# Kernel optimization log

Hardware: AMD Instinct MI355X
Metric: run time of the kernel (lower is better)

## Reference

```python
import jax, jax.numpy as jnp
import numpy as np

T, H, E, I, SI, TOP_K = 4096, 2048, 16, 1024, 4096, 1


def setup_inputs() -> dict:
    key = jax.random.key(0)
    ks = jax.random.split(key, 8)
    s_h = 1.0 / np.sqrt(H)
    s_i = 1.0 / np.sqrt(I)
    s_si = 1.0 / np.sqrt(SI)
    return {
        "hidden_states": jax.random.normal(ks[0], (T, H), jnp.float32),
        "router_w": jax.random.normal(ks[1], (E, H), jnp.float32) * s_h,
        "w_gate": jax.random.normal(ks[2], (E, H, I), jnp.float32) * s_h,
        "w_up": jax.random.normal(ks[3], (E, H, I), jnp.float32) * s_h,
        "w_down": jax.random.normal(ks[4], (E, I, H), jnp.float32) * s_i,
        "ws_gate": jax.random.normal(ks[5], (H, SI), jnp.float32) * s_h,
        "ws_up": jax.random.normal(ks[6], (H, SI), jnp.float32) * s_h,
        "ws_down": jax.random.normal(ks[7], (SI, H), jnp.float32) * s_si,
    }


def reference(hidden_states, router_w, w_gate, w_up, w_down, ws_gate, ws_up, ws_down):
    x = hidden_states  # [T, H]
    # Router: logits -> top-k -> sigmoid weights (Llama4RenormalizeMoeRoutingMethod)
    logits = jnp.einsum("th,eh->te", x, router_w)              # [T, E]
    top_vals, top_idx = jax.lax.top_k(logits, TOP_K)            # [T, K]
    weights = jax.nn.sigmoid(top_vals)                          # [T, K]
    # dispatch[t, e] = router weight if expert e selected for token t, else 0
    onehot = jax.nn.one_hot(top_idx, E, dtype=x.dtype)          # [T, K, E]
    dispatch = jnp.einsum("tke,tk->te", onehot, weights)        # [T, E]
    # Routed experts: router weight applied on input (commutes through the
    # linear gate/up projections as a per-(t,e) scalar applied before SiLU).
    g = jnp.einsum("th,ehi->tei", x, w_gate) * dispatch[:, :, None]  # [T, E, I]
    u = jnp.einsum("th,ehi->tei", x, w_up) * dispatch[:, :, None]    # [T, E, I]
    act = jax.nn.silu(g) * u                                          # [T, E, I]
    # Unselected experts contribute exactly 0 (act==0 there), so summing over
    # E in the down projection is the combine step.
    routed = jnp.einsum("tei,eih->th", act, w_down)             # [T, H]
    # Shared expert (SiLU-gated MLP on the unscaled hidden states)
    shared = (jax.nn.silu(x @ ws_gate) * (x @ ws_up)) @ ws_down  # [T, H]
    return shared + routed
```

## Files before the change

kernel.cpp:

```cpp
#include <hip/hip_runtime.h>
#include <hip/hip_bf16.h>

typedef unsigned short u16;
typedef unsigned int   u32;
typedef __attribute__((ext_vector_type(8))) short short8;
typedef __attribute__((ext_vector_type(4))) float f32x4;

#define T_TOK 4096
#define HDIM  2048
#define NEXP  16
#define IDIM  1024
#define SIDIM 4096
#define RCAP  6144
#define NTIL  48

#define O_WT      0u
#define O_EIDX    16384u
#define O_CNT     32768u
#define O_POS     32832u
#define O_PADOFF  32896u
#define O_TILEEXP 33024u
#define O_TOKROW  33280u
#define O_XBF     65536u
#define O_XSC     (O_XBF  + 2u*T_TOK*HDIM)
#define O_ACTS    (O_XSC  + 2u*RCAP*HDIM)
#define O_ACTR    (O_ACTS + 2u*T_TOK*SIDIM)
#define O_WSGT    (O_ACTR + 2u*RCAP*IDIM)
#define O_WSUT    (O_WSGT + 2u*SIDIM*HDIM)
#define O_WSDT    (O_WSUT + 2u*SIDIM*HDIM)

__device__ __forceinline__ u16 f2b(float f) {
  u32 u = __float_as_uint(f);
  u = (u + 0x7FFFu + ((u >> 16) & 1u)) >> 16;
  return (u16)u;
}

#define GLDS16(g, l) __builtin_amdgcn_global_load_lds( \
    (const __attribute__((address_space(1))) void*)(g), \
    (__attribute__((address_space(3))) void*)(l), 16, 0, 0)
#define BARX() __builtin_amdgcn_s_barrier()
#define SETPRIO(x) __builtin_amdgcn_s_setprio(x)
#define WAITVM(n) asm volatile("s_waitcnt vmcnt(" #n ")" ::: "memory")

__global__ __launch_bounds__(256) void router_k(
    const float* __restrict__ x, const float* __restrict__ rw,
    float* __restrict__ wt, int* __restrict__ eidx, int* __restrict__ cnt,
    u16* __restrict__ xbf) {
  int w = threadIdx.x >> 6, l = threadIdx.x & 63;
  int t = blockIdx.x * 4 + w;
  double acc[NEXP];
#pragma unroll
  for (int e = 0; e < NEXP; ++e) acc[e] = 0.0;
  const float* xp = x + (size_t)t * HDIM;
  u16* xo = xbf + (size_t)t * HDIM;
  for (int hb = 0; hb < HDIM; hb += 256) {
    float4 xv = *(const float4*)(xp + hb + l * 4);
    uint2 o;
    o.x = (u32)f2b(xv.x) | ((u32)f2b(xv.y) << 16);
    o.y = (u32)f2b(xv.z) | ((u32)f2b(xv.w) << 16);
    *(uint2*)(xo + hb + l * 4) = o;
#pragma unroll
    for (int e = 0; e < NEXP; ++e) {
      float4 wv = *(const float4*)(rw + (size_t)e * HDIM + hb + l * 4);
      acc[e] += (double)xv.x * wv.x + (double)xv.y * wv.y
              + (double)xv.z * wv.z + (double)xv.w * wv.w;
    }
  }
#pragma unroll
  for (int e = 0; e < NEXP; ++e) {
    double v = acc[e];
#pragma unroll
    for (int off = 32; off; off >>= 1) v += __shfl_xor(v, off, 64);
    acc[e] = v;
  }
  if (l == 0) {
    double best = acc[0]; int be = 0;
#pragma unroll
    for (int e = 1; e < NEXP; ++e) if (acc[e] > best) { best = acc[e]; be = e; }
    wt[t] = 1.0f / (1.0f + __expf(-(float)best));
    eidx[t] = be;
    atomicAdd(&cnt[be], 1);
  }
}

__global__ void scan_k(const int* __restrict__ cnt, int* __restrict__ pad_off,
                       int* __restrict__ tile_exp, int* __restrict__ pos,
                       int* __restrict__ tok_row) {
  if (threadIdx.x == 0) {
    for (int i = 0; i < 64; ++i) tile_exp[i] = -1;
    int run = 0;
    for (int e = 0; e < NEXP; ++e) {
      pad_off[e] = run;
      int pc = ((cnt[e] + 127) >> 7) << 7;
      for (int tt = run >> 7; tt < (run + pc) >> 7; ++tt) tile_exp[tt] = e;
      run += pc;
      pos[e] = 0;
    }
    pad_off[NEXP] = run;
  }
  for (int i = threadIdx.x; i < RCAP; i += 256) tok_row[i] = -1;
}

__global__ void assign_k(const int* __restrict__ eidx, const int* __restrict__ pad_off,
                         int* __restrict__ pos, int* __restrict__ tok_row) {
  int t = blockIdx.x * 256 + threadIdx.x;
  if (t >= T_TOK) return;
  int e = eidx[t];
  int r = atomicAdd(&pos[e], 1);
  tok_row[pad_off[e] + r] = t;
}

__global__ __launch_bounds__(256) void gather_k(
    const float* __restrict__ x, const float* __restrict__ wt,
    const int* __restrict__ tok_row, u16* __restrict__ xsc) {
  int g = blockIdx.x;
  int tid = threadIdx.x;
  u16* dst = xsc + (size_t)g * HDIM;
  int t = tok_row[g];
  if (t < 0) {
    uint2 z; z.x = 0u; z.y = 0u;
#pragma unroll
    for (int i = 0; i < 2; ++i) *(uint2*)(dst + i * 1024 + tid * 4) = z;
  } else {
    float s = wt[t];
    const float* src = x + (size_t)t * HDIM;
#pragma unroll
    for (int i = 0; i < 2; ++i) {
      int c = i * 1024 + tid * 4;
      float4 v = *(const float4*)(src + c);
      uint2 o;
      o.x = (u32)f2b(v.x * s) | ((u32)f2b(v.y * s) << 16);
      o.y = (u32)f2b(v.z * s) | ((u32)f2b(v.w * s) << 16);
      *(uint2*)(dst + c) = o;
    }
  }
}

__device__ __forceinline__ void conv_tile(
    const float* __restrict__ src, u16* __restrict__ dst, int K, int N,
    int bx, int ky, u32 (*lt)[36], int tid) {
  const int n0 = bx * 64, k0 = ky * 64;
  const int l = tid & 63, w = tid >> 6;
  const float* sp = src + (size_t)(k0 + w * 16) * N + n0 + l;
  u32 p[8];
#pragma unroll
  for (int i = 0; i < 8; ++i) {
    float a = sp[(size_t)(2 * i) * N];
    float b = sp[(size_t)(2 * i + 1) * N];
    p[i] = (u32)f2b(a) | ((u32)f2b(b) << 16);
  }
  *(uint4*)&lt[l][w * 8 + 0] = make_uint4(p[0], p[1], p[2], p[3]);
  *(uint4*)&lt[l][w * 8 + 4] = make_uint4(p[4], p[5], p[6], p[7]);
  __syncthreads();
  const int c = tid & 7, n2 = tid >> 3;
#pragma unroll
  for (int rnd = 0; rnd < 2; ++rnd) {
    int n = n2 + rnd * 32;
    uint4 v = *(const uint4*)&lt[n][c * 4];
    *(uint4*)(dst + (size_t)(n0 + n) * K + k0 + c * 8) = v;
  }
}

__global__ __launch_bounds__(256) void megaconv(
    const float* __restrict__ wsg, const float* __restrict__ wsu,
    const float* __restrict__ wsd, u16* wsgT, u16* wsuT, u16* wsdT) {
  __shared__ u32 lt[64][36];
  int idx = blockIdx.x, tid = threadIdx.x;
  if (idx < 2048) {
    conv_tile(wsg, wsgT, 2048, 4096, idx & 63, idx >> 6, lt, tid);
  } else if (idx < 4096) { idx -= 2048;
    conv_tile(wsu, wsuT, 2048, 4096, idx & 63, idx >> 6, lt, tid);
  } else { idx -= 4096;
    conv_tile(wsd, wsdT, 4096, 2048, idx & 31, idx >> 5, lt, tid);
  }
}


__global__ __launch_bounds__(512, 2) void gu_sh8(
    const u16* __restrict__ A, const u16* __restrict__ Bg, const u16* __restrict__ Bu,
    u16* __restrict__ act) {
  extern __shared__ u16 sm[];
  u16* As  = sm;
  u16* Bsm = sm + 32768;
  const int bid = blockIdx.x;
  const int xcd = bid & 7, bi = bid >> 3;
  const int bx = xcd * 4 + (bi & 3), by = bi >> 2;
  const int m0 = by * 256, c0 = bx * 128;
  const int tid = threadIdx.x, l = tid & 63, wid = tid >> 6;
  const int wm = wid >> 1, wn = wid & 1;

  const int cpos = tid & 3, rr = tid >> 2;
  const int gc = (cpos ^ ((rr >> 1) & 3)) * 8;
  const u16* aS0 = A + (size_t)(m0 + rr) * HDIM + gc;
  const u16* aS1 = A + (size_t)(m0 + 128 + rr) * HDIM + gc;
  const int mat = (rr >> 6) & 1;
  const u16* bbase = mat ? Bu : Bg;
  const u16* bS0 = bbase + (size_t)(c0 + (rr & 63)) * HDIM + gc;
  const u16* bS1 = bbase + (size_t)(c0 + 64 + (rr & 63)) * HDIM + gc;
  const int ld0 = tid * 8, ld1 = (512 + tid) * 8;

#define STA_G(bb, kh, koff) do { \
    GLDS16(aS0 + (koff) + (kh) * 32, As + ((bb) * 2 + (kh)) * 8192 + ld0); \
    GLDS16(aS1 + (koff) + (kh) * 32, As + ((bb) * 2 + (kh)) * 8192 + ld1); } while (0)
#define STB_G(bb, kh, koff) do { \
    GLDS16(bS0 + (koff) + (kh) * 32, Bsm + ((bb) * 2 + (kh)) * 8192 + ld0); \
    GLDS16(bS1 + (koff) + (kh) * 32, Bsm + ((bb) * 2 + (kh)) * 8192 + ld1); } while (0)

  const int fch = ((l >> 4) ^ ((l >> 1) & 3)) * 8;
  int aoff[4], boff[8];
#pragma unroll
  for (int mf = 0; mf < 4; ++mf) aoff[mf] = (wm * 64 + mf * 16 + (l & 15)) * 32 + fch;
#pragma unroll
  for (int i = 0; i < 8; ++i) {
    int v = wn * 128 + (i >> 2) * 64 + (i & 3) * 16 + (l & 15);
    boff[i] = v * 32 + fch;
  }
#define LDA_G(bb, kh) do { const u16* s_ = As + ((bb) * 2 + (kh)) * 8192; \
    af[0] = *(const short8*)(s_ + aoff[0]); af[1] = *(const short8*)(s_ + aoff[1]); \
    af[2] = *(const short8*)(s_ + aoff[2]); af[3] = *(const short8*)(s_ + aoff[3]); } while (0)
#define LDB_G(bb, kh, h, d) do { const u16* s_ = Bsm + ((bb) * 2 + (kh)) * 8192; \
    d[0] = *(const short8*)(s_ + boff[(h) * 4 + 0]); d[1] = *(const short8*)(s_ + boff[(h) * 4 + 1]); \
    d[2] = *(const short8*)(s_ + boff[(h) * 4 + 2]); d[3] = *(const short8*)(s_ + boff[(h) * 4 + 3]); } while (0)
#define MM32_G() do { SETPRIO(1); \
    _Pragma("unroll") for (int mf = 0; mf < 4; ++mf) { \
      _Pragma("unroll") for (int nf = 0; nf < 4; ++nf) \
        acc[mf][nf] = __builtin_amdgcn_mfma_f32_16x16x32_bf16(af[mf], bfrA[nf], acc[mf][nf], 0, 0, 0); \
      _Pragma("unroll") for (int nf = 0; nf < 4; ++nf) \
        acc[mf][4 + nf] = __builtin_amdgcn_mfma_f32_16x16x32_bf16(af[mf], bfrB[nf], acc[mf][4 + nf], 0, 0, 0); \
    } SETPRIO(0); } while (0)

  f32x4 acc[4][8];
#pragma unroll
  for (int i = 0; i < 4; ++i)
#pragma unroll
    for (int j = 0; j < 8; ++j)
#pragma unroll
      for (int r = 0; r < 4; ++r) acc[i][j][r] = 0.0f;
  short8 af[4], bfrA[4], bfrB[4];

  STA_G(0, 0, 0); STB_G(0, 0, 0); STA_G(0, 1, 0); STB_G(0, 1, 0);
  WAITVM(4); BARX();
  const int NT = HDIM / 64;
  for (int t = 0; t < NT - 1; ++t) {
    const int b = t & 1, nb = b ^ 1, kn = (t + 1) * 64;
    LDA_G(b, 0); LDB_G(b, 0, 0, bfrA); LDB_G(b, 0, 1, bfrB);
    STA_G(nb, 0, kn); STB_G(nb, 0, kn);
    MM32_G(); WAITVM(4); BARX();
    LDA_G(b, 1); LDB_G(b, 1, 0, bfrA); LDB_G(b, 1, 1, bfrB);
    STA_G(nb, 1, kn); STB_G(nb, 1, kn);
    MM32_G(); WAITVM(4); BARX();
  }
  { const int b = (NT - 1) & 1;
    LDA_G(b, 0); LDB_G(b, 0, 0, bfrA); LDB_G(b, 0, 1, bfrB);
    MM32_G(); WAITVM(0); BARX();
    LDA_G(b, 1); LDB_G(b, 1, 0, bfrA); LDB_G(b, 1, 1, bfrB);
    MM32_G();
  }
#pragma unroll
  for (int mf = 0; mf < 4; ++mf)
#pragma unroll
    for (int nf = 0; nf < 4; ++nf) {
      int col = c0 + wn * 64 + nf * 16 + (l & 15);
      int rowb = m0 + wm * 64 + mf * 16 + (l >> 4) * 4;
#pragma unroll
      for (int r = 0; r < 4; ++r) {
        float g = acc[mf][nf][r], u = acc[mf][4 + nf][r];
        float s = g / (1.0f + __expf(-g));
        act[(size_t)(rowb + r) * SIDIM + col] = f2b(s * u);
      }
    }
#undef STA_G
#undef STB_G
#undef LDA_G
#undef LDB_G
#undef MM32_G
}

__global__ __launch_bounds__(512, 2) void dn_sh8(
    const u16* __restrict__ A, const u16* __restrict__ B, float* __restrict__ out) {
  extern __shared__ u16 sm[];
  u16* As  = sm;
  u16* Bsm = sm + 32768;
  const int bid = blockIdx.x;
  const int xcd = bid & 7, bi = bid >> 3;
  const int bx = xcd * 2 + (bi & 1), by = bi >> 1;
  const int m0 = by * 256, c0 = bx * 128;
  const int tid = threadIdx.x, l = tid & 63, wid = tid >> 6;
  const int wm = wid >> 1, wn = wid & 1;

  const int cpos = tid & 3, rr = tid >> 2;
  const int gc = (cpos ^ ((rr >> 1) & 3)) * 8;
  const u16* aS0 = A + (size_t)(m0 + rr) * SIDIM + gc;
  const u16* aS1 = A + (size_t)(m0 + 128 + rr) * SIDIM + gc;
  const u16* bS  = B + (size_t)(c0 + rr) * SIDIM + gc;
  const int ld0 = tid * 8, ld1 = (512 + tid) * 8;

#define STA_D(bb, kh, koff) do { \
    GLDS16(aS0 + (koff) + (kh) * 32, As + ((bb) * 2 + (kh)) * 8192 + ld0); \
    GLDS16(aS1 + (koff) + (kh) * 32, As + ((bb) * 2 + (kh)) * 8192 + ld1); } while (0)
#define STB_D(bb, kh, koff) \
    GLDS16(bS + (koff) + (kh) * 32, Bsm + ((bb) * 2 + (kh)) * 4096 + ld0)

  const int fch = ((l >> 4) ^ ((l >> 1) & 3)) * 8;
  int aoff[4], boff[4];
#pragma unroll
  for (int mf = 0; mf < 4; ++mf) aoff[mf] = (wm * 64 + mf * 16 + (l & 15)) * 32 + fch;
#pragma unroll
  for (int i = 0; i < 4; ++i) {
    int v = wn * 64 + (i >> 1) * 32 + (i & 1) * 16 + (l & 15);
    boff[i] = v * 32 + fch;
  }
#define LDA_D(bb, kh) do { const u16* s_ = As + ((bb) * 2 + (kh)) * 8192; \
    af[0] = *(const short8*)(s_ + aoff[0]); af[1] = *(const short8*)(s_ + aoff[1]); \
    af[2] = *(const short8*)(s_ + aoff[2]); af[3] = *(const short8*)(s_ + aoff[3]); } while (0)
#define LDB_D(bb, kh, h, d) do { const u16* s_ = Bsm + ((bb) * 2 + (kh)) * 4096; \
    d[0] = *(const short8*)(s_ + boff[(h) * 2 + 0]); \
    d[1] = *(const short8*)(s_ + boff[(h) * 2 + 1]); } while (0)
#define MM16_D() do { SETPRIO(1); \
    _Pragma("unroll") for (int mf = 0; mf < 4; ++mf) { \
      acc[mf][0] = __builtin_amdgcn_mfma_f32_16x16x32_bf16(af[mf], bfrA[0], acc[mf][0], 0, 0, 0); \
      acc[mf][1] = __builtin_amdgcn_mfma_f32_16x16x32_bf16(af[mf], bfrA[1], acc[mf][1], 0, 0, 0); \
      acc[mf][2] = __builtin_amdgcn_mfma_f32_16x16x32_bf16(af[mf], bfrB[0], acc[mf][2], 0, 0, 0); \
      acc[mf][3] = __builtin_amdgcn_mfma_f32_16x16x32_bf16(af[mf], bfrB[1], acc[mf][3], 0, 0, 0); \
    } SETPRIO(0); } while (0)

  f32x4 acc[4][4];
#pragma unroll
  for (int i = 0; i < 4; ++i)
#pragma unroll
    for (int j = 0; j < 4; ++j)
#pragma unroll
      for (int r = 0; r < 4; ++r) acc[i][j][r] = 0.0f;
  short8 af[4], bfrA[2], bfrB[2];

  STA_D(0, 0, 0); STB_D(0, 0, 0); STA_D(0, 1, 0); STB_D(0, 1, 0);
  WAITVM(3); BARX();
  const int NT = SIDIM / 64;
  for (int t = 0; t < NT - 1; ++t) {
    const int b = t & 1, nb = b ^ 1, kn = (t + 1) * 64;
    LDA_D(b, 0); LDB_D(b, 0, 0, bfrA); LDB_D(b, 0, 1, bfrB);
    STA_D(nb, 0, kn); STB_D(nb, 0, kn);
    MM16_D(); WAITVM(3); BARX();
    LDA_D(b, 1); LDB_D(b, 1, 0, bfrA); LDB_D(b, 1, 1, bfrB);
    STA_D(nb, 1, kn); STB_D(nb, 1, kn);
    MM16_D(); WAITVM(3); BARX();
  }
  { const int b = (NT - 1) & 1;
    LDA_D(b, 0); LDB_D(b, 0, 0, bfrA); LDB_D(b, 0, 1, bfrB);
    MM16_D(); WAITVM(0); BARX();
    LDA_D(b, 1); LDB_D(b, 1, 0, bfrA); LDB_D(b, 1, 1, bfrB);
    MM16_D();
  }
#pragma unroll
  for (int mf = 0; mf < 4; ++mf)
#pragma unroll
    for (int nf = 0; nf < 4; ++nf) {
      int col = c0 + wn * 64 + (nf >> 1) * 32 + (nf & 1) * 16 + (l & 15);
      int rowb = m0 + wm * 64 + mf * 16 + (l >> 4) * 4;
#pragma unroll
      for (int r = 0; r < 4; ++r)
        out[(size_t)(rowb + r) * HDIM + col] = acc[mf][nf][r];
    }
#undef STA_D
#undef STB_D
#undef LDA_D
#undef LDB_D
#undef MM16_D
}

__global__ __launch_bounds__(256) void gu_rf(
    const u16* __restrict__ A, const float* __restrict__ Bg0, const float* __restrict__ Bu0,
    u16* __restrict__ act, const int* __restrict__ tile_exp) {
  __shared__ __align__(16) u16 As[128 * 64];
  __shared__ __align__(16) u16 Bgs[64 * 72];
  __shared__ __align__(16) u16 Bus[64 * 72];
  const int tid = threadIdx.x;
  const int l = tid & 63, w = tid >> 6;
  const int wm = w >> 1, wn = w & 1;
  const int m0 = blockIdx.y * 128, n0 = blockIdx.x * 64;
  int e = tile_exp[blockIdx.y];
  if (e < 0) return;
  size_t eo = (size_t)e * HDIM * IDIM;
  const float* Bg = Bg0 + eo;
  const float* Bu = Bu0 + eo;
  f32x4 accg[4][2], accu[4][2];
#pragma unroll
  for (int i = 0; i < 4; ++i)
#pragma unroll
    for (int j = 0; j < 2; ++j)
#pragma unroll
      for (int r = 0; r < 4; ++r) { accg[i][j][r] = 0.0f; accu[i][j][r] = 0.0f; }
  const u16* Ab = A + (size_t)m0 * HDIM;

  for (int k0 = 0; k0 < HDIM; k0 += 64) {
    __syncthreads();
#pragma unroll
    for (int j = 0; j < 4; ++j) {
      int c = j * 256 + tid, r = c >> 3, cc = c & 7;
      GLDS16(Ab + (size_t)r * HDIM + k0 + ((cc ^ (r & 7)) * 8), &As[c * 8]);
    }
    {
      const float* bp = Bg + (size_t)(k0 + w * 16) * IDIM + n0 + l;
      u16 h[16];
#pragma unroll
      for (int i = 0; i < 16; ++i) h[i] = f2b(bp[(size_t)i * IDIM]);
#pragma unroll
      for (int j = 0; j < 4; ++j) {
        uint2 v; v.x = (u32)h[4*j] | ((u32)h[4*j+1] << 16);
        v.y = (u32)h[4*j+2] | ((u32)h[4*j+3] << 16);
        *(uint2*)&Bgs[l * 72 + w * 16 + j * 4] = v;
      }
      bp = Bu + (size_t)(k0 + w * 16) * IDIM + n0 + l;
#pragma unroll
      for (int i = 0; i < 16; ++i) h[i] = f2b(bp[(size_t)i * IDIM]);
#pragma unroll
      for (int j = 0; j < 4; ++j) {
        uint2 v; v.x = (u32)h[4*j] | ((u32)h[4*j+1] << 16);
        v.y = (u32)h[4*j+2] | ((u32)h[4*j+3] << 16);
        *(uint2*)&Bus[l * 72 + w * 16 + j * 4] = v;
      }
    }
    __syncthreads();
#pragma unroll
    for (int kh = 0; kh < 2; ++kh) {
      const int q = kh * 4 + (l >> 4);
      short8 af[4];
#pragma unroll
      for (int mf = 0; mf < 4; ++mf) {
        int r = wm * 64 + mf * 16 + (l & 15);
        af[mf] = *(const short8*)&As[r * 64 + ((q ^ (r & 7)) * 8)];
      }
      short8 bgf[2], buf2[2];
#pragma unroll
      for (int nf = 0; nf < 2; ++nf) {
        int n = wn * 32 + nf * 16 + (l & 15);
        bgf[nf]  = *(const short8*)&Bgs[n * 72 + q * 8];
        buf2[nf] = *(const short8*)&Bus[n * 72 + q * 8];
      }
#pragma unroll
      for (int mf = 0; mf < 4; ++mf)
#pragma unroll
        for (int nf = 0; nf < 2; ++nf) {
          accg[mf][nf] = __builtin_amdgcn_mfma_f32_16x16x32_bf16(af[mf], bgf[nf],  accg[mf][nf], 0, 0, 0);
          accu[mf][nf] = __builtin_amdgcn_mfma_f32_16x16x32_bf16(af[mf], buf2[nf], accu[mf][nf], 0, 0, 0);
        }
    }
  }
#pragma unroll
  for (int mf = 0; mf < 4; ++mf)
#pragma unroll
    for (int nf = 0; nf < 2; ++nf) {
      int col = n0 + wn * 32 + nf * 16 + (l & 15);
#pragma unroll
      for (int r = 0; r < 4; ++r) {
        int row = m0 + wm * 64 + mf * 16 + (l >> 4) * 4 + r;
        float g = accg[mf][nf][r], u = accu[mf][nf][r];
        float s = g / (1.0f + __expf(-g));
        act[(size_t)row * IDIM + col] = f2b(s * u);
      }
    }
}

__global__ __launch_bounds__(256) void dn_rf(
    const u16* __restrict__ A, const float* __restrict__ B0, float* __restrict__ out,
    const int* __restrict__ tile_exp, const int* __restrict__ tok_row) {
  __shared__ __align__(16) u16 As[128 * 64];
  __shared__ __align__(16) u16 Bs[64 * 72];
  const int tid = threadIdx.x;
  const int l = tid & 63, w = tid >> 6;
  const int wm = w >> 1, wn = w & 1;
  const int m0 = blockIdx.y * 128, n0 = blockIdx.x * 64;
  int e = tile_exp[blockIdx.y];
  if (e < 0) return;
  const float* B = B0 + (size_t)e * IDIM * HDIM;
  f32x4 acc[4][2];
#pragma unroll
  for (int i = 0; i < 4; ++i)
#pragma unroll
    for (int j = 0; j < 2; ++j)
#pragma unroll
      for (int r = 0; r < 4; ++r) acc[i][j][r] = 0.0f;
  const u16* Ab = A + (size_t)m0 * IDIM;

  for (int k0 = 0; k0 < IDIM; k0 += 64) {
    __syncthreads();
#pragma unroll
    for (int j = 0; j < 4; ++j) {
      int c = j * 256 + tid, r = c >> 3, cc = c & 7;
      GLDS16(Ab + (size_t)r * IDIM + k0 + ((cc ^ (r & 7)) * 8), &As[c * 8]);
    }
    {
      const float* bp = B + (size_t)(k0 + w * 16) * HDIM + n0 + l;
      u16 h[16];
#pragma unroll
      for (int i = 0; i < 16; ++i) h[i] = f2b(bp[(size_t)i * HDIM]);
#pragma unroll
      for (int j = 0; j < 4; ++j) {
        uint2 v; v.x = (u32)h[4*j] | ((u32)h[4*j+1] << 16);
        v.y = (u32)h[4*j+2] | ((u32)h[4*j+3] << 16);
        *(uint2*)&Bs[l * 72 + w * 16 + j * 4] = v;
      }
    }
    __syncthreads();
#pragma unroll
    for (int kh = 0; kh < 2; ++kh) {
      const int q = kh * 4 + (l >> 4);
      short8 af[4];
#pragma unroll
      for (int mf = 0; mf < 4; ++mf) {
        int r = wm * 64 + mf * 16 + (l & 15);
        af[mf] = *(const short8*)&As[r * 64 + ((q ^ (r & 7)) * 8)];
      }
      short8 bf[2];
#pragma unroll
      for (int nf = 0; nf < 2; ++nf) {
        int n = wn * 32 + nf * 16 + (l & 15);
        bf[nf] = *(const short8*)&Bs[n * 72 + q * 8];
      }
#pragma unroll
      for (int mf = 0; mf < 4; ++mf)
#pragma unroll
        for (int nf = 0; nf < 2; ++nf)
          acc[mf][nf] = __builtin_amdgcn_mfma_f32_16x16x32_bf16(af[mf], bf[nf], acc[mf][nf], 0, 0, 0);
    }
  }
#pragma unroll
  for (int mf = 0; mf < 4; ++mf)
#pragma unroll
    for (int nf = 0; nf < 2; ++nf) {
      int col = n0 + wn * 32 + nf * 16 + (l & 15);
#pragma unroll
      for (int r = 0; r < 4; ++r) {
        int grow = m0 + wm * 64 + mf * 16 + (l >> 4) * 4 + r;
        int t = tok_row[grow];
        if (t >= 0) out[(size_t)t * HDIM + col] += acc[mf][nf][r];
      }
    }
}

extern "C" void kernel_launch(void* const* d_in, const int* in_sizes, int n_in,
                              void* d_out, int out_size, void* d_ws, size_t ws_size,
                              hipStream_t stream) {
  const float* x   = (const float*)d_in[0];
  const float* rw  = (const float*)d_in[1];
  const float* wg  = (const float*)d_in[2];
  const float* wu  = (const float*)d_in[3];
  const float* wd  = (const float*)d_in[4];
  const float* wsg = (const float*)d_in[5];
  const float* wsu = (const float*)d_in[6];
  const float* wsd = (const float*)d_in[7];
  float* out = (float*)d_out;
  char* ws = (char*)d_ws;

  float* wt     = (float*)(ws + O_WT);
  int* eidx     = (int*)(ws + O_EIDX);
  int* cnt      = (int*)(ws + O_CNT);
  int* pos      = (int*)(ws + O_POS);
  int* pad_off  = (int*)(ws + O_PADOFF);
  int* tile_exp = (int*)(ws + O_TILEEXP);
  int* tok_row  = (int*)(ws + O_TOKROW);
  u16* xbf      = (u16*)(ws + O_XBF);
  u16* xsc      = (u16*)(ws + O_XSC);
  u16* acts     = (u16*)(ws + O_ACTS);
  u16* actr     = (u16*)(ws + O_ACTR);
  u16* wsgT     = (u16*)(ws + O_WSGT);
  u16* wsuT     = (u16*)(ws + O_WSUT);
  u16* wsdT     = (u16*)(ws + O_WSDT);

  hipFuncSetAttribute((const void*)gu_sh8, hipFuncAttributeMaxDynamicSharedMemorySize, 131072);
  hipFuncSetAttribute((const void*)dn_sh8, hipFuncAttributeMaxDynamicSharedMemorySize, 98304);

  hipMemsetAsync(ws + O_CNT, 0, 128, stream);
  megaconv<<<6144, 256, 0, stream>>>(wsg, wsu, wsd, wsgT, wsuT, wsdT);
  router_k<<<T_TOK / 4, 256, 0, stream>>>(x, rw, wt, eidx, cnt, xbf);
  scan_k<<<1, 256, 0, stream>>>(cnt, pad_off, tile_exp, pos, tok_row);
  assign_k<<<T_TOK / 256, 256, 0, stream>>>(eidx, pad_off, pos, tok_row);
  gather_k<<<RCAP, 256, 0, stream>>>(x, wt, tok_row, xsc);

  gu_sh8<<<512, 512, 131072, stream>>>(xbf, wsgT, wsuT, acts);
  gu_rf<<<dim3(IDIM / 64, NTIL), 256, 0, stream>>>(xsc, wg, wu, actr, tile_exp);
  dn_sh8<<<256, 512, 98304, stream>>>(acts, wsdT, out);
  dn_rf<<<dim3(HDIM / 64, NTIL), 256, 0, stream>>>(actr, wd, out, tile_exp, tok_row);
}
```

Measured before the change: 569.9 us.

## Software-pipeline routed expert GEMMs with double-buffered A and register-prefetched B

Both routed-expert kernels, gate/up and down, now double-buffer the A tile in LDS. The fp32 weight loads for the next K-step are issued into registers before the current step's MFMAs, so global latency overlaps with compute instead of sitting between two __syncthreads. Synchronisation uses explicit vmcnt/lgkmcnt waits, raw barriers and sched_barrier, and wave priority is raised around the MFMA block. This costs more LDS and registers per block, which could lower occupancy.

```diff
diff --git a/kernel.cpp b/kernel.cpp
--- a/kernel.cpp
+++ b/kernel.cpp
@@ -41,6 +41,8 @@
 #define BARX() __builtin_amdgcn_s_barrier()
 #define SETPRIO(x) __builtin_amdgcn_s_setprio(x)
 #define WAITVM(n) asm volatile("s_waitcnt vmcnt(" #n ")" ::: "memory")
+#define WAITLGKM0() asm volatile("s_waitcnt lgkmcnt(0)" ::: "memory")
+#define SCHEDB() __builtin_amdgcn_sched_barrier(0)
 
 __global__ __launch_bounds__(256) void router_k(
     const float* __restrict__ x, const float* __restrict__ rw,
@@ -368,10 +370,11 @@
 #undef MM16_D
 }
 
+
 __global__ __launch_bounds__(256) void gu_rf(
     const u16* __restrict__ A, const float* __restrict__ Bg0, const float* __restrict__ Bu0,
     u16* __restrict__ act, const int* __restrict__ tile_exp) {
-  __shared__ __align__(16) u16 As[128 * 64];
+  __shared__ __align__(16) u16 As[2][128 * 64];
   __shared__ __align__(16) u16 Bgs[64 * 72];
   __shared__ __align__(16) u16 Bus[64 * 72];
   const int tid = threadIdx.x;
@@ -381,8 +384,8 @@
   int e = tile_exp[blockIdx.y];
   if (e < 0) return;
   size_t eo = (size_t)e * HDIM * IDIM;
-  const float* Bg = Bg0 + eo;
-  const float* Bu = Bu0 + eo;
+  const float* Bgp = Bg0 + eo + n0 + l;
+  const float* Bup = Bu0 + eo + n0 + l;
   f32x4 accg[4][2], accu[4][2];
 #pragma unroll
   for (int i = 0; i < 4; ++i)
@@ -391,36 +394,39 @@
 #pragma unroll
       for (int r = 0; r < 4; ++r) { accg[i][j][r] = 0.0f; accu[i][j][r] = 0.0f; }
   const u16* Ab = A + (size_t)m0 * HDIM;
-
-  for (int k0 = 0; k0 < HDIM; k0 += 64) {
-    __syncthreads();
-#pragma unroll
-    for (int j = 0; j < 4; ++j) {
-      int c = j * 256 + tid, r = c >> 3, cc = c & 7;
-      GLDS16(Ab + (size_t)r * HDIM + k0 + ((cc ^ (r & 7)) * 8), &As[c * 8]);
-    }
-    {
-      const float* bp = Bg + (size_t)(k0 + w * 16) * IDIM + n0 + l;
-      u16 h[16];
-#pragma unroll
-      for (int i = 0; i < 16; ++i) h[i] = f2b(bp[(size_t)i * IDIM]);
-#pragma unroll
-      for (int j = 0; j < 4; ++j) {
-        uint2 v; v.x = (u32)h[4*j] | ((u32)h[4*j+1] << 16);
-        v.y = (u32)h[4*j+2] | ((u32)h[4*j+3] << 16);
-        *(uint2*)&Bgs[l * 72 + w * 16 + j * 4] = v;
-      }
-      bp = Bu + (size_t)(k0 + w * 16) * IDIM + n0 + l;
-#pragma unroll
-      for (int i = 0; i < 16; ++i) h[i] = f2b(bp[(size_t)i * IDIM]);
-#pragma unroll
-      for (int j = 0; j < 4; ++j) {
-        uint2 v; v.x = (u32)h[4*j] | ((u32)h[4*j+1] << 16);
-        v.y = (u32)h[4*j+2] | ((u32)h[4*j+3] << 16);
-        *(uint2*)&Bus[l * 72 + w * 16 + j * 4] = v;
-      }
-    }
-    __syncthreads();
+  float bg[16], bu[16];
+
+#define STAGE_A_R(bb, k0) do { \
+    _Pragma("unroll") for (int j = 0; j < 4; ++j) { \
+      int c_ = j * 256 + tid, r_ = c_ >> 3, cc_ = c_ & 7; \
+      GLDS16(Ab + (size_t)r_ * HDIM + (k0) + ((cc_ ^ (r_ & 7)) * 8), &As[bb][c_ * 8]); } } while (0)
+#define LOADB_R(k0) do { \
+    _Pragma("unroll") for (int i = 0; i < 16; ++i) { \
+      bg[i] = Bgp[(size_t)((k0) + w * 16 + i) * IDIM]; \
+      bu[i] = Bup[(size_t)((k0) + w * 16 + i) * IDIM]; } } while (0)
+#define WRITEB_R() do { \
+    _Pragma("unroll") for (int j = 0; j < 4; ++j) { \
+      uint2 v_; v_.x = (u32)f2b(bg[4*j]) | ((u32)f2b(bg[4*j+1]) << 16); \
+      v_.y = (u32)f2b(bg[4*j+2]) | ((u32)f2b(bg[4*j+3]) << 16); \
+      *(uint2*)&Bgs[l * 72 + w * 16 + j * 4] = v_; \
+      uint2 u_; u_.x = (u32)f2b(bu[4*j]) | ((u32)f2b(bu[4*j+1]) << 16); \
+      u_.y = (u32)f2b(bu[4*j+2]) | ((u32)f2b(bu[4*j+3]) << 16); \
+      *(uint2*)&Bus[l * 72 + w * 16 + j * 4] = u_; } } while (0)
+
+  STAGE_A_R(0, 0);
+  SCHEDB();
+  LOADB_R(0);
+  WAITVM(32); BARX();
+  const int NT = HDIM / 64;
+  for (int t = 0; t < NT; ++t) {
+    const int b = t & 1, nb = b ^ 1;
+    WRITEB_R();
+    if (t + 1 < NT) {
+      STAGE_A_R(nb, (t + 1) * 64);
+      SCHEDB();
+      LOADB_R((t + 1) * 64);
+    }
+    WAITLGKM0(); BARX();
 #pragma unroll
     for (int kh = 0; kh < 2; ++kh) {
       const int q = kh * 4 + (l >> 4);
@@ -428,7 +434,7 @@
 #pragma unroll
       for (int mf = 0; mf < 4; ++mf) {
         int r = wm * 64 + mf * 16 + (l & 15);
-        af[mf] = *(const short8*)&As[r * 64 + ((q ^ (r & 7)) * 8)];
+        af[mf] = *(const short8*)&As[b][r * 64 + ((q ^ (r & 7)) * 8)];
       }
       short8 bgf[2], buf2[2];
 #pragma unroll
@@ -437,6 +443,7 @@
         bgf[nf]  = *(const short8*)&Bgs[n * 72 + q * 8];
         buf2[nf] = *(const short8*)&Bus[n * 72 + q * 8];
       }
+      SETPRIO(1);
 #pragma unroll
       for (int mf = 0; mf < 4; ++mf)
 #pragma unroll
@@ -444,7 +451,9 @@
           accg[mf][nf] = __builtin_amdgcn_mfma_f32_16x16x32_bf16(af[mf], bgf[nf],  accg[mf][nf], 0, 0, 0);
           accu[mf][nf] = __builtin_amdgcn_mfma_f32_16x16x32_bf16(af[mf], buf2[nf], accu[mf][nf], 0, 0, 0);
         }
-    }
+      SETPRIO(0);
+    }
+    WAITVM(32); BARX();
   }
 #pragma unroll
   for (int mf = 0; mf < 4; ++mf)
@@ -459,12 +468,15 @@
         act[(size_t)row * IDIM + col] = f2b(s * u);
       }
     }
+#undef STAGE_A_R
+#undef LOADB_R
+#undef WRITEB_R
 }
 
 __global__ __launch_bounds__(256) void dn_rf(
     const u16* __restrict__ A, const float* __restrict__ B0, float* __restrict__ out,
     const int* __restrict__ tile_exp, const int* __restrict__ tok_row) {
-  __shared__ __align__(16) u16 As[128 * 64];
+  __shared__ __align__(16) u16 As[2][128 * 64];
   __shared__ __align__(16) u16 Bs[64 * 72];
   const int tid = threadIdx.x;
   const int l = tid & 63, w = tid >> 6;
@@ -472,7 +484,7 @@
   const int m0 = blockIdx.y * 128, n0 = blockIdx.x * 64;
   int e = tile_exp[blockIdx.y];
   if (e < 0) return;
-  const float* B = B0 + (size_t)e * IDIM * HDIM;
+  const float* Bp = B0 + (size_t)e * IDIM * HDIM + n0 + l;
   f32x4 acc[4][2];
 #pragma unroll
   for (int i = 0; i < 4; ++i)
@@ -481,27 +493,35 @@
 #pragma unroll
       for (int r = 0; r < 4; ++r) acc[i][j][r] = 0.0f;
   const u16* Ab = A + (size_t)m0 * IDIM;
-
-  for (int k0 = 0; k0 < IDIM; k0 += 64) {
-    __syncthreads();
-#pragma unroll
-    for (int j = 0; j < 4; ++j) {
-      int c = j * 256 + tid, r = c >> 3, cc = c & 7;
-      GLDS16(Ab + (size_t)r * IDIM + k0 + ((cc ^ (r & 7)) * 8), &As[c * 8]);
-    }
-    {
-      const float* bp = B + (size_t)(k0 + w * 16) * HDIM + n0 + l;
-      u16 h[16];
-#pragma unroll
-      for (int i = 0; i < 16; ++i) h[i] = f2b(bp[(size_t)i * HDIM]);
-#pragma unroll
-      for (int j = 0; j < 4; ++j) {
-        uint2 v; v.x = (u32)h[4*j] | ((u32)h[4*j+1] << 16);
-        v.y = (u32)h[4*j+2] | ((u32)h[4*j+3] << 16);
-        *(uint2*)&Bs[l * 72 + w * 16 + j * 4] = v;
-      }
-    }
-    __syncthreads();
+  float bb[16];
+
+#define STAGE_A_D(bbuf, k0) do { \
+    _Pragma("unroll") for (int j = 0; j < 4; ++j) { \
+      int c_ = j * 256 + tid, r_ = c_ >> 3, cc_ = c_ & 7; \
+      GLDS16(Ab + (size_t)r_ * IDIM + (k0) + ((cc_ ^ (r_ & 7)) * 8), &As[bbuf][c_ * 8]); } } while (0)
+#define LOADB_D(k0) do { \
+    _Pragma("unroll") for (int i = 0; i < 16; ++i) \
+      bb[i] = Bp[(size_t)((k0) + w * 16 + i) * HDIM]; } while (0)
+#define WRITEB_D() do { \
+    _Pragma("unroll") for (int j = 0; j < 4; ++j) { \
+      uint2 v_; v_.x = (u32)f2b(bb[4*j]) | ((u32)f2b(bb[4*j+1]) << 16); \
+      v_.y = (u32)f2b(bb[4*j+2]) | ((u32)f2b(bb[4*j+3]) << 16); \
+      *(uint2*)&Bs[l * 72 + w * 16 + j * 4] = v_; } } while (0)
+
+  STAGE_A_D(0, 0);
+  SCHEDB();
+  LOADB_D(0);
+  WAITVM(16); BARX();
+  const int NT = IDIM / 64;
+  for (int t = 0; t < NT; ++t) {
+    const int b = t & 1, nb = b ^ 1;
+    WRITEB_D();
+    if (t + 1 < NT) {
+      STAGE_A_D(nb, (t + 1) * 64);
+      SCHEDB();
+      LOADB_D((t + 1) * 64);
+    }
+    WAITLGKM0(); BARX();
 #pragma unroll
     for (int kh = 0; kh < 2; ++kh) {
       const int q = kh * 4 + (l >> 4);
@@ -509,7 +529,7 @@
 #pragma unroll
       for (int mf = 0; mf < 4; ++mf) {
         int r = wm * 64 + mf * 16 + (l & 15);
-        af[mf] = *(const short8*)&As[r * 64 + ((q ^ (r & 7)) * 8)];
+        af[mf] = *(const short8*)&As[b][r * 64 + ((q ^ (r & 7)) * 8)];
       }
       short8 bf[2];
 #pragma unroll
@@ -517,12 +537,15 @@
         int n = wn * 32 + nf * 16 + (l & 15);
         bf[nf] = *(const short8*)&Bs[n * 72 + q * 8];
       }
+      SETPRIO(1);
 #pragma unroll
       for (int mf = 0; mf < 4; ++mf)
 #pragma unroll
         for (int nf = 0; nf < 2; ++nf)
           acc[mf][nf] = __builtin_amdgcn_mfma_f32_16x16x32_bf16(af[mf], bf[nf], acc[mf][nf], 0, 0, 0);
-    }
+      SETPRIO(0);
+    }
+    WAITVM(16); BARX();
   }
 #pragma unroll
   for (int mf = 0; mf < 4; ++mf)
@@ -536,6 +559,9 @@
         if (t >= 0) out[(size_t)t * HDIM + col] += acc[mf][nf][r];
       }
     }
+#undef STAGE_A_D
+#undef LOADB_D
+#undef WRITEB_D
 }
 
 extern "C" void kernel_launch(void* const* d_in, const int* in_sizes, int n_in,
```

Result: slower. 607.1 us (+6.5%).
